# Performance work log

Measured on AMD Instinct MI355X. Metric: run time of the kernel, lower is better.

The kernel has to match this reference:

```python
import jax, jax.numpy as jnp
import numpy as np
import math

THETA = 10000.0

def apply_rope(x):
    # x: [B, H, S, D] with D even; interleaved even/odd rotation
    B, H, S, D = x.shape
    dim_half = D // 2
    freq_idx = jnp.arange(dim_half, dtype=jnp.float32)
    inv_freq = jnp.exp(-math.log(THETA) * freq_idx * 2.0 / D)  # [D/2]
    pos = jnp.arange(S, dtype=jnp.float32)
    angles = pos[:, None] * inv_freq[None, :]      # [S, D/2]
    cos = jnp.cos(angles)[None, None]              # [1,1,S,D/2]
    sin = jnp.sin(angles)[None, None]
    x_even = x[..., ::2]
    x_odd = x[..., 1::2]
    r_even = x_even * cos - x_odd * sin
    r_odd = x_odd * cos + x_even * sin
    return jnp.stack([r_even, r_odd], axis=-1).reshape(B, H, S, D)

def setup_inputs() -> dict:
    key = jax.random.key(0)
    ks = jax.random.split(key, 5)
    B, S, E = 2, 2048, 1024
    std = 0.02
    inp = {
        "hidden_states": jax.random.normal(ks[0], (B, S, E), dtype=jnp.float32),
        "Wq": jax.random.normal(ks[1], (E, E), dtype=jnp.float32) * std,
        "bq": jnp.zeros((E,), dtype=jnp.float32),
        "Wk": jax.random.normal(ks[2], (E, E), dtype=jnp.float32) * std,
        "bk": jnp.zeros((E,), dtype=jnp.float32),
        "Wv": jax.random.normal(ks[3], (E, E), dtype=jnp.float32) * std,
        "bv": jnp.zeros((E,), dtype=jnp.float32),
        "Wo": jax.random.normal(ks[4], (E, E), dtype=jnp.float32) * std,
        "bo": jnp.zeros((E,), dtype=jnp.float32),
    }
    return inp

def reference(hidden_states, Wq, bq, Wk, bk, Wv, bv, Wo, bo):
    NUM_HEADS = 16
    B, S, E = hidden_states.shape
    D = E // NUM_HEADS
    scale = 1.0 / math.sqrt(D)

    def proj(W, b):
        # torch Linear: x @ W.T + b; then [B,S,H,D] -> [B,H,S,D]
        y = hidden_states @ W.T + b
        return y.reshape(B, S, NUM_HEADS, D).transpose(0, 2, 1, 3)

    q = apply_rope(proj(Wq, bq))
    k = apply_rope(proj(Wk, bk))
    v = proj(Wv, bv)

    scores = jnp.einsum("bhqd,bhkd->bhqk", q, k) * scale
    attn = jax.nn.softmax(scores, axis=-1)
    out = jnp.einsum("bhqk,bhkd->bhqd", attn, v)  # [B,H,S,D]
    out = out.transpose(0, 2, 1, 3).reshape(B, S, E)
    return out @ Wo.T + bo  # dropout: eval mode (identity)
```

## Files before the change

kernel.cpp:

```cpp
#include <hip/hip_runtime.h>
#include <math.h>

#define B_ 2
#define S_ 2048
#define E_ 1024
#define H_ 16
#define D_ 64
#define M_ (B_*S_)
#define PT 40

typedef short bf16x8 __attribute__((ext_vector_type(8)));
typedef float f32x4 __attribute__((ext_vector_type(4)));
typedef unsigned short u16x4 __attribute__((ext_vector_type(4)));

__device__ __forceinline__ unsigned short f2bf(float f) {
    unsigned int u = __builtin_bit_cast(unsigned int, f);
    u += 0x7FFFu + ((u >> 16) & 1u);
    return (unsigned short)(u >> 16);
}
__device__ __forceinline__ f32x4 mfma16(bf16x8 a, bf16x8 b, f32x4 c) {
    return __builtin_amdgcn_mfma_f32_16x16x32_bf16(a, b, c, 0, 0, 0);
}
__device__ __forceinline__ bf16x8 cvt8(const float* p) {
    f32x4 lo = *(const f32x4*)p;
    f32x4 hi = *(const f32x4*)(p + 4);
    bf16x8 r;
#pragma unroll
    for (int e = 0; e < 4; e++) { r[e] = (short)f2bf(lo[e]); r[e + 4] = (short)f2bf(hi[e]); }
    return r;
}

__global__ __launch_bounds__(256, 3) void qkv_rope_kernel(
    const float* __restrict__ X,
    const float* __restrict__ Wq, const float* __restrict__ Wk,
    const float* __restrict__ Wv,
    const float* __restrict__ bq, const float* __restrict__ bk,
    const float* __restrict__ bv,
    unsigned short* __restrict__ Qo, unsigned short* __restrict__ Ko,
    unsigned short* __restrict__ Vo)
{
    __shared__ __align__(16) unsigned char lds_raw[128 * 132 * 2];
    unsigned short* As = (unsigned short*)lds_raw;
    unsigned short* Bs = (unsigned short*)(lds_raw + 128 * PT * 2);
    unsigned short* Cs = (unsigned short*)lds_raw;

    const int t = threadIdx.x;
    const int w = t >> 6, lane = t & 63, quad = lane >> 4, l16 = lane & 15;
    const int wr = (w >> 1) * 64, wc = (w & 1) * 64;
    const int n0 = blockIdx.x * 128, m0 = blockIdx.y * 128;
    const int z = blockIdx.z;
    const float* W    = (z == 0) ? Wq : (z == 1) ? Wk : Wv;
    const float* bias = (z == 0) ? bq : (z == 1) ? bk : bv;

    const int r4 = t >> 2, c8 = (t & 3) * 8;
    const int st = r4 * PT + c8;
    const float* Ag = X + (size_t)(m0 + r4) * E_ + c8;
    const float* Bg = W + (size_t)(n0 + r4) * E_ + c8;

    f32x4 zero = {0.f, 0.f, 0.f, 0.f};
    f32x4 acc[4][4];
#pragma unroll
    for (int i = 0; i < 4; i++)
#pragma unroll
        for (int j = 0; j < 4; j++) acc[i][j] = zero;

    for (int kt = 0; kt < E_; kt += 32) {
        bf16x8 a0 = cvt8(Ag + kt);
        bf16x8 a1 = cvt8(Ag + 64 * E_ + kt);
        bf16x8 b0 = cvt8(Bg + kt);
        bf16x8 b1 = cvt8(Bg + 64 * E_ + kt);
        __syncthreads();
        *(bf16x8*)&As[st]           = a0;
        *(bf16x8*)&As[st + 64 * PT] = a1;
        *(bf16x8*)&Bs[st]           = b0;
        *(bf16x8*)&Bs[st + 64 * PT] = b1;
        __syncthreads();
        bf16x8 af[4], bfr[4];
#pragma unroll
        for (int i = 0; i < 4; i++)
            af[i] = *(const bf16x8*)&As[(wr + i * 16 + l16) * PT + quad * 8];
#pragma unroll
        for (int j = 0; j < 4; j++)
            bfr[j] = *(const bf16x8*)&Bs[(wc + j * 16 + l16) * PT + quad * 8];
#pragma unroll
        for (int i = 0; i < 4; i++)
#pragma unroll
            for (int j = 0; j < 4; j++)
                acc[i][j] = mfma16(af[i], bfr[j], acc[i][j]);
    }

    __syncthreads();
    const int seg = quad;
    if (z < 2) {
        const float C = -0.41524101186091903f;
        const float INV2PI = 0.15915494309189535f;
#pragma unroll
        for (int j = 0; j < 4; j++) {
            int n_local = wc + j * 16 + l16;
            int n = n0 + n_local;
            int d = n & 63, f = d >> 1;
            float inv_rev = exp2f(C * (float)f) * INV2PI;
            float bvv = bias[n];
            float sgn = (d & 1) ? 1.f : -1.f;
#pragma unroll
            for (int i = 0; i < 4; i++) {
                int mb = wr + i * 16 + quad * 4;
#pragma unroll
                for (int r = 0; r < 4; r++) {
                    int m = m0 + mb + r;
                    int s = m & (S_ - 1);
                    float val = acc[i][j][r] + bvv;
                    float oth = __shfl_xor(val, 1);
                    float rev = (float)s * inv_rev;
                    float fr = rev - rintf(rev);
                    float sn = __builtin_amdgcn_sinf(fr);
                    float cs = __builtin_amdgcn_cosf(fr);
                    Cs[(mb + r) * 132 + n_local] = f2bf(val * cs + sgn * oth * sn);
                }
            }
        }
        __syncthreads();
        unsigned short* Out = (z == 0) ? Qo : Ko;
        const int btok = m0 >> 11;
        const int half = seg & 1;
#pragma unroll
        for (int it = 0; it < 16; it++) {
            int m_local = it * 8 + w * 2 + (seg >> 1);
            int s = (m0 + m_local) & (S_ - 1);
            int h = (n0 + half * 64) >> 6;
            u16x4 v = *(const u16x4*)&Cs[m_local * 132 + half * 64 + l16 * 4];
            *(u16x4*)&Out[(((size_t)btok * H_ + h) * S_ + s) * D_ + l16 * 4] = v;
        }
    } else {
#pragma unroll
        for (int j = 0; j < 4; j++) {
            int n_local = wc + j * 16 + l16;
            float bvv = bias[n0 + n_local];
#pragma unroll
            for (int i = 0; i < 4; i++) {
                int mb = wr + i * 16 + quad * 4;
#pragma unroll
                for (int r = 0; r < 4; r++)
                    Cs[n_local * 132 + mb + r] = f2bf(acc[i][j][r] + bvv);
            }
        }
        __syncthreads();
        const int btok = m0 >> 11;
        const int s0 = m0 & (S_ - 1);
        const int half = seg & 1;
#pragma unroll
        for (int it = 0; it < 16; it++) {
            int n_local = it * 8 + w * 2 + (seg >> 1);
            int n = n0 + n_local;
            int h = n >> 6, d = n & 63;
            u16x4 v = *(const u16x4*)&Cs[n_local * 132 + half * 64 + l16 * 4];
            *(u16x4*)&Vo[(((size_t)btok * H_ + h) * D_ + d) * S_ + s0 + half * 64 + l16 * 4] = v;
        }
    }
}

__global__ __launch_bounds__(256, 4) void attn_kernel(
    const unsigned short* __restrict__ Q, const unsigned short* __restrict__ K,
    const unsigned short* __restrict__ Vt, unsigned short* __restrict__ ctx)
{
    __shared__ unsigned short Ks[2][64 * PT];
    __shared__ unsigned short Vs[2][64 * PT];
    __shared__ unsigned short Ps[4][16 * 72];
    const int t = threadIdx.x;
    const int w = t >> 6, lane = t & 63, quad = lane >> 4, l16 = lane & 15;
    const int bh = blockIdx.y;
    const int q0 = blockIdx.x * 64 + w * 16;

    const unsigned short* Qg = Q + ((size_t)bh * S_ + q0) * D_;
    bf16x8 qf[2];
#pragma unroll
    for (int ks = 0; ks < 2; ks++)
        qf[ks] = *(const bf16x8*)(Qg + (size_t)l16 * 64 + ks * 32 + quad * 8);

    bf16x8 ones;
#pragma unroll
    for (int e = 0; e < 8; e++) ones[e] = (short)0x3F80;

    f32x4 zero = {0.f, 0.f, 0.f, 0.f};
    f32x4 acc_o[4];
    f32x4 acc_l = zero;
#pragma unroll
    for (int j = 0; j < 4; j++) acc_o[j] = zero;

    const int r4 = t >> 2, c8v = (t & 3) * 8;
    const int st = r4 * PT + c8v;
    const unsigned short* Kg0 = K + (size_t)bh * S_ * D_;
    const unsigned short* Vg0 = Vt + (size_t)bh * D_ * S_;

    for (int kt = 0; kt < S_; kt += 64) {
        const unsigned short* Kg = Kg0 + (size_t)(kt + r4) * 64 + c8v;
        const unsigned short* Vg = Vg0 + (size_t)r4 * S_ + kt + c8v;
        bf16x8 k0 = *(const bf16x8*)(Kg);
        bf16x8 k1 = *(const bf16x8*)(Kg + 32);
        bf16x8 v0 = *(const bf16x8*)(Vg);
        bf16x8 v1 = *(const bf16x8*)(Vg + 32);
        __syncthreads();
        *(bf16x8*)&Ks[0][st] = k0;
        *(bf16x8*)&Ks[1][st] = k1;
        *(bf16x8*)&Vs[0][st] = v0;
        *(bf16x8*)&Vs[1][st] = v1;
        __syncthreads();

        f32x4 sc[4];
#pragma unroll
        for (int j = 0; j < 4; j++) sc[j] = zero;
#pragma unroll
        for (int ks = 0; ks < 2; ks++) {
#pragma unroll
            for (int j = 0; j < 4; j++) {
                bf16x8 kf = *(const bf16x8*)&Ks[ks][(j * 16 + l16) * PT + quad * 8];
                sc[j] = mfma16(qf[ks], kf, sc[j]);
            }
        }
#pragma unroll
        for (int j = 0; j < 4; j++)
#pragma unroll
            for (int r = 0; r < 4; r++) {
                float p = __expf(sc[j][r] * 0.125f);
                Ps[w][(quad * 4 + r) * 72 + j * 16 + l16] = f2bf(p);
            }
#pragma unroll
        for (int ks = 0; ks < 2; ks++) {
            bf16x8 pf = *(const bf16x8*)&Ps[w][l16 * 72 + ks * 32 + quad * 8];
#pragma unroll
            for (int jd = 0; jd < 4; jd++) {
                bf16x8 vf = *(const bf16x8*)&Vs[ks][(jd * 16 + l16) * PT + quad * 8];
                acc_o[jd] = mfma16(pf, vf, acc_o[jd]);
            }
            acc_l = mfma16(pf, ones, acc_l);
        }
    }

    const int b = bh >> 4, h = bh & 15;
    f32x4 rl;
#pragma unroll
    for (int r = 0; r < 4; r++) rl[r] = 1.0f / acc_l[r];
#pragma unroll
    for (int jd = 0; jd < 4; jd++)
#pragma unroll
        for (int r = 0; r < 4; r++) {
            int qrow = q0 + quad * 4 + r;
            int col = h * 64 + jd * 16 + l16;
            ctx[((size_t)b * S_ + qrow) * E_ + col] = f2bf(acc_o[jd][r] * rl[r]);
        }
}

__global__ __launch_bounds__(256, 2) void out_kernel(
    const unsigned short* __restrict__ Cx, const float* __restrict__ Wo,
    const float* __restrict__ bo, float* __restrict__ out)
{
    __shared__ unsigned short As[128 * PT];
    __shared__ unsigned short Bs[64 * PT];
    const int t = threadIdx.x;
    const int w = t >> 6, lane = t & 63, quad = lane >> 4, l16 = lane & 15;
    const int m0 = blockIdx.y * 128, n0 = blockIdx.x * 64;
    const int wr = w * 32;
    const int r4 = t >> 2, c8 = (t & 3) * 8;
    const int st = r4 * PT + c8;
    const unsigned short* Ag = Cx + (size_t)(m0 + r4) * E_ + c8;
    const float*          Bg = Wo + (size_t)(n0 + (r4 & 63)) * E_ + c8;

    f32x4 zero = {0.f, 0.f, 0.f, 0.f};
    f32x4 acc[2][4];
#pragma unroll
    for (int i = 0; i < 2; i++)
#pragma unroll
        for (int j = 0; j < 4; j++) acc[i][j] = zero;

    for (int kt = 0; kt < E_; kt += 32) {
        bf16x8 a0 = *(const bf16x8*)(Ag + kt);
        bf16x8 a1 = *(const bf16x8*)(Ag + 64 * E_ + kt);
        bf16x8 b0 = cvt8(Bg + kt);
        __syncthreads();
        *(bf16x8*)&As[st]           = a0;
        *(bf16x8*)&As[st + 64 * PT] = a1;
        *(bf16x8*)&Bs[st]           = b0;
        __syncthreads();
        bf16x8 af[2], bfr[4];
#pragma unroll
        for (int i = 0; i < 2; i++)
            af[i] = *(const bf16x8*)&As[(wr + i * 16 + l16) * PT + quad * 8];
#pragma unroll
        for (int j = 0; j < 4; j++)
            bfr[j] = *(const bf16x8*)&Bs[(j * 16 + l16) * PT + quad * 8];
#pragma unroll
        for (int i = 0; i < 2; i++)
#pragma unroll
            for (int j = 0; j < 4; j++)
                acc[i][j] = mfma16(af[i], bfr[j], acc[i][j]);
    }

#pragma unroll
    for (int j = 0; j < 4; j++) {
        int n = n0 + j * 16 + l16;
        float bvv = bo[n];
#pragma unroll
        for (int i = 0; i < 2; i++) {
            int mrow = m0 + wr + i * 16 + quad * 4;
#pragma unroll
            for (int r = 0; r < 4; r++)
                out[(size_t)(mrow + r) * E_ + n] = acc[i][j][r] + bvv;
        }
    }
}

extern "C" void kernel_launch(void* const* d_in, const int* in_sizes, int n_in,
                              void* d_out, int out_size, void* d_ws, size_t ws_size,
                              hipStream_t stream) {
    const float* X  = (const float*)d_in[0];
    const float* Wq = (const float*)d_in[1];
    const float* bq = (const float*)d_in[2];
    const float* Wk = (const float*)d_in[3];
    const float* bk = (const float*)d_in[4];
    const float* Wv = (const float*)d_in[5];
    const float* bv = (const float*)d_in[6];
    const float* Wo = (const float*)d_in[7];
    const float* bo = (const float*)d_in[8];
    float* outp = (float*)d_out;

    const size_t TN = (size_t)B_ * H_ * S_ * D_;
    if (ws_size < 4 * TN * sizeof(unsigned short)) return;

    unsigned short* Qb = (unsigned short*)d_ws;
    unsigned short* Kb = Qb + TN;
    unsigned short* Vb = Kb + TN;
    unsigned short* Cx = Vb + TN;

    qkv_rope_kernel<<<dim3(E_ / 128, M_ / 128, 3), 256, 0, stream>>>(
        X, Wq, Wk, Wv, bq, bk, bv, Qb, Kb, Vb);
    attn_kernel<<<dim3(S_ / 64, B_ * H_), 256, 0, stream>>>(Qb, Kb, Vb, Cx);
    out_kernel<<<dim3(E_ / 64, M_ / 128), 256, 0, stream>>>(Cx, Wo, bo, outp);
}
```

Baseline: 223.3 us.

## Grow attention block to 128 queries with 8 waves sharing K/V tiles

Doubles the attention block to 512 threads covering 128 query rows, so each staged 64-key K/V tile in LDS is reused by eight waves instead of four. Each thread now loads one bf16x8 of K and one of V instead of two each. The LDS row padding is removed (pitch 40 to 32), which may add bank conflicts on the fragment reads. The softmax exponent switches to a native exp2 with the log2(e) factor folded into the scale. Fewer blocks and removed padding trade occupancy and LDS conflict risk for less global traffic and fewer barriers per query row.

```diff
diff --git a/kernel.cpp b/kernel.cpp
--- a/kernel.cpp
+++ b/kernel.cpp
@@ -7,7 +7,7 @@
 #define H_ 16
 #define D_ 64
 #define M_ (B_*S_)
-#define PT 40
+#define PT 32
 
 typedef short bf16x8 __attribute__((ext_vector_type(8)));
 typedef float f32x4 __attribute__((ext_vector_type(4)));
@@ -159,17 +159,17 @@
     }
 }
 
-__global__ __launch_bounds__(256, 4) void attn_kernel(
+__global__ __launch_bounds__(512, 4) void attn_kernel(
     const unsigned short* __restrict__ Q, const unsigned short* __restrict__ K,
     const unsigned short* __restrict__ Vt, unsigned short* __restrict__ ctx)
 {
-    __shared__ unsigned short Ks[2][64 * PT];
-    __shared__ unsigned short Vs[2][64 * PT];
-    __shared__ unsigned short Ps[4][16 * 72];
+    __shared__ unsigned short Ks[2][64 * 32];
+    __shared__ unsigned short Vs[2][64 * 32];
+    __shared__ unsigned short Ps[8][16 * 72];
     const int t = threadIdx.x;
     const int w = t >> 6, lane = t & 63, quad = lane >> 4, l16 = lane & 15;
     const int bh = blockIdx.y;
-    const int q0 = blockIdx.x * 64 + w * 16;
+    const int q0 = blockIdx.x * 128 + w * 16;
 
     const unsigned short* Qg = Q + ((size_t)bh * S_ + q0) * D_;
     bf16x8 qf[2];
@@ -187,23 +187,22 @@
 #pragma unroll
     for (int j = 0; j < 4; j++) acc_o[j] = zero;
 
-    const int r4 = t >> 2, c8v = (t & 3) * 8;
-    const int st = r4 * PT + c8v;
+    const int r8 = t >> 3;
+    const int c8 = (t & 7) * 8;
+    const int stKV = (c8 >> 5) * 2048 + r8 * 32 + (c8 & 31);
+    unsigned short* KsF = &Ks[0][0];
+    unsigned short* VsF = &Vs[0][0];
     const unsigned short* Kg0 = K + (size_t)bh * S_ * D_;
     const unsigned short* Vg0 = Vt + (size_t)bh * D_ * S_;
 
+    const float SCL = 0.18033688011f;
+
     for (int kt = 0; kt < S_; kt += 64) {
-        const unsigned short* Kg = Kg0 + (size_t)(kt + r4) * 64 + c8v;
-        const unsigned short* Vg = Vg0 + (size_t)r4 * S_ + kt + c8v;
-        bf16x8 k0 = *(const bf16x8*)(Kg);
-        bf16x8 k1 = *(const bf16x8*)(Kg + 32);
-        bf16x8 v0 = *(const bf16x8*)(Vg);
-        bf16x8 v1 = *(const bf16x8*)(Vg + 32);
-        __syncthreads();
-        *(bf16x8*)&Ks[0][st] = k0;
-        *(bf16x8*)&Ks[1][st] = k1;
-        *(bf16x8*)&Vs[0][st] = v0;
-        *(bf16x8*)&Vs[1][st] = v1;
+        bf16x8 k0 = *(const bf16x8*)(Kg0 + (size_t)(kt + r8) * 64 + c8);
+        bf16x8 v0 = *(const bf16x8*)(Vg0 + (size_t)r8 * S_ + kt + c8);
+        __syncthreads();
+        *(bf16x8*)&KsF[stKV] = k0;
+        *(bf16x8*)&VsF[stKV] = v0;
         __syncthreads();
 
         f32x4 sc[4];
@@ -213,7 +212,7 @@
         for (int ks = 0; ks < 2; ks++) {
 #pragma unroll
             for (int j = 0; j < 4; j++) {
-                bf16x8 kf = *(const bf16x8*)&Ks[ks][(j * 16 + l16) * PT + quad * 8];
+                bf16x8 kf = *(const bf16x8*)&Ks[ks][(j * 16 + l16) * 32 + quad * 8];
                 sc[j] = mfma16(qf[ks], kf, sc[j]);
             }
         }
@@ -221,7 +220,7 @@
         for (int j = 0; j < 4; j++)
 #pragma unroll
             for (int r = 0; r < 4; r++) {
-                float p = __expf(sc[j][r] * 0.125f);
+                float p = __builtin_amdgcn_exp2f(sc[j][r] * SCL);
                 Ps[w][(quad * 4 + r) * 72 + j * 16 + l16] = f2bf(p);
             }
 #pragma unroll
@@ -229,7 +228,7 @@
             bf16x8 pf = *(const bf16x8*)&Ps[w][l16 * 72 + ks * 32 + quad * 8];
 #pragma unroll
             for (int jd = 0; jd < 4; jd++) {
-                bf16x8 vf = *(const bf16x8*)&Vs[ks][(jd * 16 + l16) * PT + quad * 8];
+                bf16x8 vf = *(const bf16x8*)&Vs[ks][(jd * 16 + l16) * 32 + quad * 8];
                 acc_o[jd] = mfma16(pf, vf, acc_o[jd]);
             }
             acc_l = mfma16(pf, ones, acc_l);
@@ -333,6 +332,6 @@
 
     qkv_rope_kernel<<<dim3(E_ / 128, M_ / 128, 3), 256, 0, stream>>>(
         X, Wq, Wk, Wv, bq, bk, bv, Qb, Kb, Vb);
-    attn_kernel<<<dim3(S_ / 64, B_ * H_), 256, 0, stream>>>(Qb, Kb, Vb, Cx);
+    attn_kernel<<<dim3(S_ / 128, B_ * H_), 512, 0, stream>>>(Qb, Kb, Vb, Cx);
     out_kernel<<<dim3(E_ / 64, M_ / 128), 256, 0, stream>>>(Cx, Wo, bo, outp);
 }
```

Result: faster. 218.9 us (-2.0%).
